# Performance work log

Measured on AMD Instinct MI355X. Metric: run time of the kernel, lower is better.

## Reference

```python
import jax, jax.numpy as jnp
import numpy as np

B, T, F, H, O = 64, 4096, 100, 200, 1


def setup_inputs() -> dict:
    key = jax.random.key(0)
    ks = jax.random.split(key, 7)
    s_i = 1.0 / np.sqrt(F)
    s_h = 1.0 / np.sqrt(H)
    return {
        "x": jax.random.normal(ks[0], (B, T, F), dtype=jnp.float32),
        # input-to-hidden weights for gates [r, z, n], concatenated: [F, 3H]
        "Wi": jax.random.uniform(ks[1], (F, 3 * H), jnp.float32, -s_i, s_i),
        "bi": jnp.zeros((3 * H,), jnp.float32),
        # hidden-to-hidden weights for gates [r, z, n]: [H, 3H] (no bias for r,z in flax GRUCell)
        "Wh": jax.random.uniform(ks[2], (H, 3 * H), jnp.float32, -s_h, s_h),
        "bhn": jnp.zeros((H,), jnp.float32),  # bias only on the h->n projection
        "Wo": jax.random.uniform(ks[3], (H, O), jnp.float32, -s_h, s_h),
        "bo": jnp.zeros((O,), jnp.float32),
    }


def _gru_forward(x, Wi, bi, Wh, bhn):
    # Precompute input projections for all timesteps: [B, T, 3H]
    gi_all = jnp.einsum("btf,fg->btg", x, Wi) + bi
    gi_all = jnp.transpose(gi_all, (1, 0, 2))  # [T, B, 3H]
    h0 = jnp.zeros((x.shape[0], Wh.shape[0]), x.dtype)

    def step(h, gi):
        hh = h @ Wh  # [B, 3H]
        r = jax.nn.sigmoid(gi[:, :H] + hh[:, :H])
        z = jax.nn.sigmoid(gi[:, H:2 * H] + hh[:, H:2 * H])
        n = jnp.tanh(gi[:, 2 * H:] + r * (hh[:, 2 * H:] + bhn))
        h_new = (1.0 - z) * n + z * h  # flax GRUCell convention
        return h_new, h_new

    _, hs = jax.lax.scan(step, h0, gi_all)  # hs: [T, B, H]
    return jnp.transpose(hs, (1, 0, 2))  # [B, T, H]


def reference(x, Wi, bi, Wh, bhn, Wo, bo):
    hs = _gru_forward(x, Wi, bi, Wh, bhn)
    return jnp.einsum("bth,ho->bto", hs, Wo) + bo  # [B, T, O]
```

## Files before the change

kernel.cpp:

```cpp
#include <hip/hip_runtime.h>
#include <cstdint>

#define B_  64
#define T_  4096
#define F_  100
#define H_  200
#define G_  600
#define KH_ 104
#define SMEM_PAD 86016

typedef _Float16 half2_t __attribute__((ext_vector_type(2)));

#define LDS_BARRIER() do {                                  \
    __builtin_amdgcn_sched_barrier(0);                      \
    asm volatile("s_waitcnt lgkmcnt(0)" ::: "memory");      \
    __builtin_amdgcn_s_barrier();                           \
    __builtin_amdgcn_sched_barrier(0);                      \
} while (0)

__device__ __forceinline__ float sigmoid_(float x) {
    return __builtin_amdgcn_rcpf(1.0f + __expf(-x));
}
__device__ __forceinline__ float tanh_(float x) {
    float e = __expf(-2.0f * x);
    return (1.0f - e) * __builtin_amdgcn_rcpf(1.0f + e);
}

__device__ __forceinline__ float fdot2_(half2_t a, half2_t b, float c) {
#if __has_builtin(__builtin_amdgcn_fdot2)
    return __builtin_amdgcn_fdot2(a, b, c, false);
#else
    return fmaf((float)a.x, (float)b.x, fmaf((float)a.y, (float)b.y, c));
#endif
}

__device__ __forceinline__ float dpp_xor1_add(float x) {
    int y = __builtin_amdgcn_update_dpp(0, __float_as_int(x), 0xB1, 0xF, 0xF, true);
    return x + __int_as_float(y);
}

__global__ void prep_whp(const float* __restrict__ Wh, half2_t* __restrict__ whp) {
    int i = blockIdx.x * 256 + threadIdx.x;
    if (i < KH_ * G_) {
        int k = i / G_, c = i - k * G_;
        half2_t v;
        v.x = (k < 100) ? (_Float16)Wh[(2 * k) * G_ + c] : (_Float16)0.f;
        v.y = (k < 100) ? (_Float16)Wh[(2 * k + 1) * G_ + c] : (_Float16)0.f;
        whp[i] = v;
    }
}

__device__ __forceinline__
void gi_body(char* smem, const float* __restrict__ x, const float* __restrict__ Wi,
             const float* __restrict__ bi, float* __restrict__ gi,
             int t0, int TC, int blk) {
    float* xT = (float*)smem;
    int tid = threadIdx.x;
    int row0 = blk * 64;
    int b    = row0 / TC;
    int tc0  = row0 - b * TC;
    const float* xrow = x + ((size_t)b * T_ + t0 + tc0) * F_;
    for (int i = tid; i < 64 * F_; i += 640) {
        int r = i / F_, f = i - r * F_;
        xT[f * 68 + r] = xrow[i];
    }
    __syncthreads();
    int col = tid < G_ ? tid : G_ - 1;
    float acc[64];
    #pragma unroll
    for (int r = 0; r < 64; ++r) acc[r] = 0.f;
    for (int f = 0; f < F_; ++f) {
        float wi = Wi[f * G_ + col];
        const float4* xf = (const float4*)&xT[f * 68];
        #pragma unroll
        for (int q = 0; q < 16; ++q) {
            float4 v = xf[q];
            acc[4*q+0] = fmaf(v.x, wi, acc[4*q+0]);
            acc[4*q+1] = fmaf(v.y, wi, acc[4*q+1]);
            acc[4*q+2] = fmaf(v.z, wi, acc[4*q+2]);
            acc[4*q+3] = fmaf(v.w, wi, acc[4*q+3]);
        }
    }
    if (tid < G_) {
        float bv = bi[col];
        float* grow = gi + (size_t)row0 * G_ + col;
        #pragma unroll 4
        for (int r = 0; r < 64; ++r) grow[(size_t)r * G_] = acc[r] + bv;
    }
}

__device__ __forceinline__
void scan_body(char* smem, const float* __restrict__ gi, const half2_t* __restrict__ whp,
               const float* __restrict__ bhn, _Float16* __restrict__ hs,
               float* __restrict__ hstate, int TC, int first, int b) {
    _Float16* h_h  = (_Float16*)smem;
    float*    A_lds = (float*)(smem + 448);
    float*    Hn_lds = (float*)(smem + 2848);
    int tid = threadIdx.x;
    int p = tid >> 1;
    int s = tid & 1;
    if (p >= 300) p = 299;
    int c0 = p;
    int c1 = p + 300;

    half2_t wa[52], wb[52];
    #pragma unroll
    for (int j = 0; j < 52; ++j) {
        wa[j] = whp[(52 * s + j) * G_ + c0];
        wb[j] = whp[(52 * s + j) * G_ + c1];
    }
    float bhn_r = (c1 >= 2*H_) ? bhn[c1 - 2*H_] : 0.f;

    float hj = 0.f;
    if (tid < H_) {
        hj = first ? 0.f : hstate[b * H_ + tid];
        h_h[tid] = (_Float16)hj;
    }
    if (tid >= H_ && tid < 208) h_h[tid] = (_Float16)0.f;
    __syncthreads();

    const float* girow = gi + (size_t)b * TC * G_;
    _Float16* hsb = hs + (size_t)b * TC * H_;

    float g0 = 0.f, g1 = 0.f;
    if (s == 0) { g0 = girow[c0]; g1 = girow[c1]; }
    for (int tc = 0; tc < TC; ++tc) {
        float g0n = 0.f, g1n = 0.f;
        if (s == 0 && tc + 1 < TC) {
            g0n = girow[(size_t)(tc + 1) * G_ + c0];
            g1n = girow[(size_t)(tc + 1) * G_ + c1];
        }
        float a0 = 0.f, a1 = 0.f, a2 = 0.f, a3 = 0.f;
        float b0 = 0.f, b1 = 0.f, b2 = 0.f, b3 = 0.f;
        const float4* h4 = (const float4*)(h_h + 104 * s);
        #pragma unroll
        for (int q = 0; q < 13; ++q) {
            float4 hv = h4[q];
            half2_t* hp = (half2_t*)&hv;
            a0 = fdot2_(hp[0], wa[4*q+0], a0);
            a1 = fdot2_(hp[1], wa[4*q+1], a1);
            a2 = fdot2_(hp[2], wa[4*q+2], a2);
            a3 = fdot2_(hp[3], wa[4*q+3], a3);
            b0 = fdot2_(hp[0], wb[4*q+0], b0);
            b1 = fdot2_(hp[1], wb[4*q+1], b1);
            b2 = fdot2_(hp[2], wb[4*q+2], b2);
            b3 = fdot2_(hp[3], wb[4*q+3], b3);
        }
        float accA = dpp_xor1_add((a0 + a1) + (a2 + a3));
        float accB = dpp_xor1_add((b0 + b1) + (b2 + b3));
        if (s == 0) {
            A_lds[c0] = g0 + accA;
            if (c1 < 2*H_) {
                A_lds[c1] = g1 + accB;
            } else {
                A_lds[c1] = g1;
                Hn_lds[c1 - 2*H_] = accB + bhn_r;
            }
        }
        LDS_BARRIER();
        if (tid < H_) {
            float r = sigmoid_(A_lds[tid]);
            float z = sigmoid_(A_lds[H_ + tid]);
            float n = tanh_(A_lds[2*H_ + tid] + r * Hn_lds[tid]);
            hj = n + z * (hj - n);
            h_h[tid] = (_Float16)hj;
            hsb[(size_t)tc * H_ + tid] = (_Float16)hj;
        }
        LDS_BARRIER();
        g0 = g0n; g1 = g1n;
    }
    if (tid < H_) hstate[b * H_ + tid] = hj;
}

__device__ __forceinline__
void out_body(const _Float16* __restrict__ hs, const float* __restrict__ Wo,
              const float* __restrict__ bo, float* __restrict__ out,
              int t0, int TC, int blk) {
    int r = blk * 640 + threadIdx.x;
    if (r >= B_ * TC) return;
    int b = r / TC, tc = r - b * TC;
    const float4* h4 = (const float4*)(hs + (size_t)r * H_);
    float acc = 0.f;
    #pragma unroll
    for (int q = 0; q < 25; ++q) {
        float4 v = h4[q];
        const _Float16* hp = (const _Float16*)&v;
        #pragma unroll
        for (int j = 0; j < 8; ++j)
            acc = fmaf((float)hp[j], Wo[q * 8 + j], acc);
    }
    out[(size_t)b * T_ + t0 + tc] = acc + bo[0];
}

__global__ __launch_bounds__(640, 1)
void fused_kernel(const float* __restrict__ x, const float* __restrict__ Wi,
                  const float* __restrict__ bi,
                  const float* __restrict__ gi_scan, float* __restrict__ gi_next,
                  const half2_t* __restrict__ whp, const float* __restrict__ bhn,
                  _Float16* __restrict__ hs_w, const _Float16* __restrict__ hs_r,
                  float* __restrict__ hstate,
                  const float* __restrict__ Wo, const float* __restrict__ bo,
                  float* __restrict__ out,
                  int c, int nc, int TC) {
    __shared__ __align__(16) char smem[SMEM_PAD];
    int blk = blockIdx.x;
    int gi_blocks = (B_ * TC) / 64;
    if (blk < 64) {
        scan_body(smem, gi_scan, whp, bhn, hs_w, hstate, TC, c == 0, blk);
    } else if (blk < 64 + gi_blocks) {
        if (c + 1 < nc)
            gi_body(smem, x, Wi, bi, gi_next, (c + 1) * TC, TC, blk - 64);
    } else {
        if (c >= 1)
            out_body(hs_r, Wo, bo, out, (c - 1) * TC, TC, blk - 64 - gi_blocks);
    }
}

__global__ __launch_bounds__(640, 1)
void gi_kernel(const float* __restrict__ x, const float* __restrict__ Wi,
               const float* __restrict__ bi, float* __restrict__ gi,
               int t0, int TC) {
    __shared__ __align__(16) char smem[F_ * 68 * 4];
    gi_body(smem, x, Wi, bi, gi, t0, TC, blockIdx.x);
}

__global__ __launch_bounds__(256, 4)
void outproj_kernel(const _Float16* __restrict__ hs, const float* __restrict__ Wo,
                    const float* __restrict__ bo, float* __restrict__ out,
                    int t0, int TC) {
    int r = blockIdx.x * 256 + threadIdx.x;
    if (r >= B_ * TC) return;
    int b = r / TC, tc = r - b * TC;
    const float4* h4 = (const float4*)(hs + (size_t)r * H_);
    float acc = 0.f;
    #pragma unroll
    for (int q = 0; q < 25; ++q) {
        float4 v = h4[q];
        const _Float16* hp = (const _Float16*)&v;
        #pragma unroll
        for (int j = 0; j < 8; ++j)
            acc = fmaf((float)hp[j], Wo[q * 8 + j], acc);
    }
    out[(size_t)b * T_ + t0 + tc] = acc + bo[0];
}

extern "C" void kernel_launch(void* const* d_in, const int* in_sizes, int n_in,
                              void* d_out, int out_size, void* d_ws, size_t ws_size,
                              hipStream_t stream) {
    const float* x   = (const float*)d_in[0];
    const float* Wi  = (const float*)d_in[1];
    const float* bi  = (const float*)d_in[2];
    const float* Wh  = (const float*)d_in[3];
    const float* bhn = (const float*)d_in[4];
    const float* Wo  = (const float*)d_in[5];
    const float* bo  = (const float*)d_in[6];
    float* out = (float*)d_out;

    const size_t hstate_b = (size_t)B_ * H_ * sizeof(float);
    const size_t whp_b    = (size_t)KH_ * G_ * sizeof(half2_t);
    int TC = 512;
    while (TC > 64 &&
           2 * (size_t)B_ * TC * (G_ * 4 + H_ * 2) + hstate_b + whp_b > ws_size)
        TC >>= 1;
    int nc = T_ / TC;
    char* p = (char*)d_ws;
    const size_t gi_b = (size_t)B_ * TC * G_ * sizeof(float);
    const size_t hs_b = (size_t)B_ * TC * H_ * sizeof(_Float16);
    float*    gi0    = (float*)p;            p += gi_b;
    float*    gi1    = (float*)p;            p += gi_b;
    _Float16* hs0    = (_Float16*)p;         p += hs_b;
    _Float16* hs1    = (_Float16*)p;         p += hs_b;
    float*    hstate = (float*)p;            p += hstate_b;
    half2_t*  whp    = (half2_t*)p;

    prep_whp<<<dim3((KH_ * G_ + 255) / 256), dim3(256), 0, stream>>>(Wh, whp);

    int gi_blocks  = (B_ * TC) / 64;
    int out_blocks = (B_ * TC + 639) / 640;
    int grid = 64 + gi_blocks + out_blocks;

    gi_kernel<<<dim3(gi_blocks), dim3(640), 0, stream>>>(x, Wi, bi, gi0, 0, TC);

    for (int c = 0; c < nc; ++c) {
        float*    gi_s = (c & 1) ? gi1 : gi0;
        float*    gi_w = (c & 1) ? gi0 : gi1;
        _Float16* hs_w = (c & 1) ? hs1 : hs0;
        _Float16* hs_r = (c & 1) ? hs0 : hs1;
        fused_kernel<<<dim3(grid), dim3(640), 0, stream>>>(
            x, Wi, bi, gi_s, gi_w, whp, bhn, hs_w, hs_r, hstate,
            Wo, bo, out, c, nc, TC);
    }
    _Float16* hs_last = ((nc - 1) & 1) ? hs1 : hs0;
    outproj_kernel<<<dim3((B_ * TC + 255) / 256), dim3(256), 0, stream>>>(
        hs_last, Wo, bo, out, (nc - 1) * TC, TC);
}
```

Baseline: 4.665 ms.

## Process two batch sequences per scan block sharing register-resident weights

Each scan block now advances two batch rows at once, reusing the same register-held Wh weights for both matvecs, which halves the scan block count from 64 to 32. The goal is to free compute units for the overlapped gi and output-projection work, and to amortise barrier and weight costs over two sequences. The trade-off is that each block's per-timestep critical path roughly doubles in dot-product work, so the serial recurrence may become longer.

```diff
diff --git a/kernel.cpp b/kernel.cpp
--- a/kernel.cpp
+++ b/kernel.cpp
@@ -90,13 +90,17 @@
 }
 
 __device__ __forceinline__
-void scan_body(char* smem, const float* __restrict__ gi, const half2_t* __restrict__ whp,
-               const float* __restrict__ bhn, _Float16* __restrict__ hs,
-               float* __restrict__ hstate, int TC, int first, int b) {
-    _Float16* h_h  = (_Float16*)smem;
-    float*    A_lds = (float*)(smem + 448);
-    float*    Hn_lds = (float*)(smem + 2848);
+void scan_body2(char* smem, const float* __restrict__ gi, const half2_t* __restrict__ whp,
+                const float* __restrict__ bhn, _Float16* __restrict__ hs,
+                float* __restrict__ hstate, int TC, int first, int blk) {
+    _Float16* h0  = (_Float16*)smem;
+    _Float16* h1  = (_Float16*)(smem + 448);
+    float*    A0  = (float*)(smem + 896);
+    float*    A1  = (float*)(smem + 3296);
+    float*    Hn0 = (float*)(smem + 5696);
+    float*    Hn1 = (float*)(smem + 6496);
     int tid = threadIdx.x;
+    int bA = 2 * blk, bB = 2 * blk + 1;
     int p = tid >> 1;
     int s = tid & 1;
     if (p >= 300) p = 299;
@@ -111,65 +115,111 @@
     }
     float bhn_r = (c1 >= 2*H_) ? bhn[c1 - 2*H_] : 0.f;
 
-    float hj = 0.f;
+    float hjA = 0.f, hjB = 0.f;
     if (tid < H_) {
-        hj = first ? 0.f : hstate[b * H_ + tid];
-        h_h[tid] = (_Float16)hj;
-    }
-    if (tid >= H_ && tid < 208) h_h[tid] = (_Float16)0.f;
+        hjA = first ? 0.f : hstate[bA * H_ + tid];
+        h0[tid] = (_Float16)hjA;
+    }
+    if (tid >= H_ && tid < 208) h0[tid] = (_Float16)0.f;
+    if (tid >= 320 && tid < 320 + H_) {
+        int e = tid - 320;
+        hjB = first ? 0.f : hstate[bB * H_ + e];
+        h1[e] = (_Float16)hjB;
+    }
+    if (tid >= 320 + H_ && tid < 320 + 208) h1[tid - 320] = (_Float16)0.f;
     __syncthreads();
 
-    const float* girow = gi + (size_t)b * TC * G_;
-    _Float16* hsb = hs + (size_t)b * TC * H_;
-
-    float g0 = 0.f, g1 = 0.f;
-    if (s == 0) { g0 = girow[c0]; g1 = girow[c1]; }
+    const float* girA = gi + (size_t)bA * TC * G_;
+    const float* girB = gi + (size_t)bB * TC * G_;
+    _Float16* hsbA = hs + (size_t)bA * TC * H_;
+    _Float16* hsbB = hs + (size_t)bB * TC * H_;
+
+    float gA0 = 0.f, gA1 = 0.f, gB0 = 0.f, gB1 = 0.f;
+    if (s == 0) {
+        gA0 = girA[c0]; gA1 = girA[c1];
+        gB0 = girB[c0]; gB1 = girB[c1];
+    }
     for (int tc = 0; tc < TC; ++tc) {
-        float g0n = 0.f, g1n = 0.f;
+        float gA0n = 0.f, gA1n = 0.f, gB0n = 0.f, gB1n = 0.f;
         if (s == 0 && tc + 1 < TC) {
-            g0n = girow[(size_t)(tc + 1) * G_ + c0];
-            g1n = girow[(size_t)(tc + 1) * G_ + c1];
-        }
-        float a0 = 0.f, a1 = 0.f, a2 = 0.f, a3 = 0.f;
-        float b0 = 0.f, b1 = 0.f, b2 = 0.f, b3 = 0.f;
-        const float4* h4 = (const float4*)(h_h + 104 * s);
-        #pragma unroll
-        for (int q = 0; q < 13; ++q) {
-            float4 hv = h4[q];
-            half2_t* hp = (half2_t*)&hv;
-            a0 = fdot2_(hp[0], wa[4*q+0], a0);
-            a1 = fdot2_(hp[1], wa[4*q+1], a1);
-            a2 = fdot2_(hp[2], wa[4*q+2], a2);
-            a3 = fdot2_(hp[3], wa[4*q+3], a3);
-            b0 = fdot2_(hp[0], wb[4*q+0], b0);
-            b1 = fdot2_(hp[1], wb[4*q+1], b1);
-            b2 = fdot2_(hp[2], wb[4*q+2], b2);
-            b3 = fdot2_(hp[3], wb[4*q+3], b3);
-        }
-        float accA = dpp_xor1_add((a0 + a1) + (a2 + a3));
-        float accB = dpp_xor1_add((b0 + b1) + (b2 + b3));
+            const float* nA = girA + (size_t)(tc + 1) * G_;
+            const float* nB = girB + (size_t)(tc + 1) * G_;
+            gA0n = nA[c0]; gA1n = nA[c1];
+            gB0n = nB[c0]; gB1n = nB[c1];
+        }
+        float x0 = 0.f, x1 = 0.f, x2 = 0.f, x3 = 0.f;
+        float y0 = 0.f, y1 = 0.f, y2 = 0.f, y3 = 0.f;
+        {
+            const float4* h4 = (const float4*)(h0 + 104 * s);
+            #pragma unroll
+            for (int q = 0; q < 13; ++q) {
+                float4 hv = h4[q];
+                half2_t* hp = (half2_t*)&hv;
+                x0 = fdot2_(hp[0], wa[4*q+0], x0);
+                x1 = fdot2_(hp[1], wa[4*q+1], x1);
+                x2 = fdot2_(hp[2], wa[4*q+2], x2);
+                x3 = fdot2_(hp[3], wa[4*q+3], x3);
+                y0 = fdot2_(hp[0], wb[4*q+0], y0);
+                y1 = fdot2_(hp[1], wb[4*q+1], y1);
+                y2 = fdot2_(hp[2], wb[4*q+2], y2);
+                y3 = fdot2_(hp[3], wb[4*q+3], y3);
+            }
+        }
+        float accA0 = dpp_xor1_add((x0 + x1) + (x2 + x3));
+        float accB0 = dpp_xor1_add((y0 + y1) + (y2 + y3));
+        x0 = 0.f; x1 = 0.f; x2 = 0.f; x3 = 0.f;
+        y0 = 0.f; y1 = 0.f; y2 = 0.f; y3 = 0.f;
+        {
+            const float4* h4 = (const float4*)(h1 + 104 * s);
+            #pragma unroll
+            for (int q = 0; q < 13; ++q) {
+                float4 hv = h4[q];
+                half2_t* hp = (half2_t*)&hv;
+                x0 = fdot2_(hp[0], wa[4*q+0], x0);
+                x1 = fdot2_(hp[1], wa[4*q+1], x1);
+                x2 = fdot2_(hp[2], wa[4*q+2], x2);
+                x3 = fdot2_(hp[3], wa[4*q+3], x3);
+                y0 = fdot2_(hp[0], wb[4*q+0], y0);
+                y1 = fdot2_(hp[1], wb[4*q+1], y1);
+                y2 = fdot2_(hp[2], wb[4*q+2], y2);
+                y3 = fdot2_(hp[3], wb[4*q+3], y3);
+            }
+        }
+        float accA1 = dpp_xor1_add((x0 + x1) + (x2 + x3));
+        float accB1 = dpp_xor1_add((y0 + y1) + (y2 + y3));
         if (s == 0) {
-            A_lds[c0] = g0 + accA;
+            A0[c0] = gA0 + accA0;
+            A1[c0] = gB0 + accA1;
             if (c1 < 2*H_) {
-                A_lds[c1] = g1 + accB;
+                A0[c1] = gA1 + accB0;
+                A1[c1] = gB1 + accB1;
             } else {
-                A_lds[c1] = g1;
-                Hn_lds[c1 - 2*H_] = accB + bhn_r;
+                A0[c1] = gA1;  Hn0[c1 - 2*H_] = accB0 + bhn_r;
+                A1[c1] = gB1;  Hn1[c1 - 2*H_] = accB1 + bhn_r;
             }
         }
         LDS_BARRIER();
         if (tid < H_) {
-            float r = sigmoid_(A_lds[tid]);
-            float z = sigmoid_(A_lds[H_ + tid]);
-            float n = tanh_(A_lds[2*H_ + tid] + r * Hn_lds[tid]);
-            hj = n + z * (hj - n);
-            h_h[tid] = (_Float16)hj;
-            hsb[(size_t)tc * H_ + tid] = (_Float16)hj;
+            float r = sigmoid_(A0[tid]);
+            float z = sigmoid_(A0[H_ + tid]);
+            float n = tanh_(A0[2*H_ + tid] + r * Hn0[tid]);
+            hjA = n + z * (hjA - n);
+            h0[tid] = (_Float16)hjA;
+            hsbA[(size_t)tc * H_ + tid] = (_Float16)hjA;
+        } else if (tid >= 320 && tid < 320 + H_) {
+            int e = tid - 320;
+            float r = sigmoid_(A1[e]);
+            float z = sigmoid_(A1[H_ + e]);
+            float n = tanh_(A1[2*H_ + e] + r * Hn1[e]);
+            hjB = n + z * (hjB - n);
+            h1[e] = (_Float16)hjB;
+            hsbB[(size_t)tc * H_ + e] = (_Float16)hjB;
         }
         LDS_BARRIER();
-        g0 = g0n; g1 = g1n;
-    }
-    if (tid < H_) hstate[b * H_ + tid] = hj;
+        gA0 = gA0n; gA1 = gA1n; gB0 = gB0n; gB1 = gB1n;
+    }
+    if (tid < H_) hstate[bA * H_ + tid] = hjA;
+    if (tid >= 320 && tid < 320 + H_) hstate[bB * H_ + tid - 320] = hjB;
 }
 
 __device__ __forceinline__
@@ -205,14 +255,14 @@
     __shared__ __align__(16) char smem[SMEM_PAD];
     int blk = blockIdx.x;
     int gi_blocks = (B_ * TC) / 64;
-    if (blk < 64) {
-        scan_body(smem, gi_scan, whp, bhn, hs_w, hstate, TC, c == 0, blk);
-    } else if (blk < 64 + gi_blocks) {
+    if (blk < 32) {
+        scan_body2(smem, gi_scan, whp, bhn, hs_w, hstate, TC, c == 0, blk);
+    } else if (blk < 32 + gi_blocks) {
         if (c + 1 < nc)
-            gi_body(smem, x, Wi, bi, gi_next, (c + 1) * TC, TC, blk - 64);
+            gi_body(smem, x, Wi, bi, gi_next, (c + 1) * TC, TC, blk - 32);
     } else {
         if (c >= 1)
-            out_body(hs_r, Wo, bo, out, (c - 1) * TC, TC, blk - 64 - gi_blocks);
+            out_body(hs_r, Wo, bo, out, (c - 1) * TC, TC, blk - 32 - gi_blocks);
     }
 }
 
@@ -277,7 +327,7 @@
 
     int gi_blocks  = (B_ * TC) / 64;
     int out_blocks = (B_ * TC + 639) / 640;
-    int grid = 64 + gi_blocks + out_blocks;
+    int grid = 32 + gi_blocks + out_blocks;
 
     gi_kernel<<<dim3(gi_blocks), dim3(640), 0, stream>>>(x, Wi, bi, gi0, 0, TC);
 
```

Result: slower. 8.110 ms (+73.8%).
